# Kernel optimization log

Measured on AMD Instinct MI355X. Metric: run time of the kernel, lower is better.

## Reference

```python
import jax, jax.numpy as jnp
import numpy as np

N = 100_000      # nodes
M = 200_000      # hyperedges
E = 1_000_000    # incidence pairs
D_IN = 64
HEADS, D_OUT = 8, 16   # linear out = 8*16 = 128


def setup_inputs() -> dict:
    key = jax.random.key(0)
    k = jax.random.split(key, 7)
    X = jax.random.normal(k[0], (N, D_IN), dtype=jnp.float32)
    vertex = jax.random.randint(k[1], (E,), 0, N, dtype=jnp.int32)
    edges = jax.random.randint(k[2], (E,), 0, M, dtype=jnp.int32)
    dege = jax.random.uniform(k[3], (M, 1), dtype=jnp.float32)
    degv = jax.random.uniform(k[4], (N, 1), dtype=jnp.float32)
    W = jax.random.normal(k[5], (D_IN, HEADS * D_OUT), dtype=jnp.float32) / np.sqrt(D_IN)
    b = jax.random.normal(k[6], (HEADS * D_OUT,), dtype=jnp.float32) * 0.01
    return {"X": X, "vertex": vertex, "edges": edges, "dege": dege, "degv": degv, "W": W, "b": b}


def reference(X, vertex, edges, dege, degv, W, b):
    n_nodes = X.shape[0]
    n_edges = dege.shape[0]
    # vertex -> hyperedge aggregation (first_aggregate = 'mean')
    Xve = X[vertex]                                               # [E, D]
    sums = jax.ops.segment_sum(Xve, edges, num_segments=n_edges)  # [M, D]
    counts = jax.ops.segment_sum(jnp.ones((edges.shape[0],), X.dtype), edges, num_segments=n_edges)
    Xe = sums / jnp.maximum(counts, 1.0)[:, None]                 # empty edges -> 0
    Xe = Xe * dege
    # hyperedge -> vertex aggregation (sum)
    Xev = Xe[edges]                                               # [E, D]
    Xv = jax.ops.segment_sum(Xev, vertex, num_segments=n_nodes)   # [N, D]
    Xv = Xv * degv
    # normalize_l2: row norm is computed on a DETACHED tensor in torch
    rownorm = jnp.linalg.norm(jax.lax.stop_gradient(Xv), axis=1, keepdims=True)
    scale = jnp.where(rownorm > 0, 1.0 / rownorm, 0.0)
    Xn = Xv * scale
    return Xn @ W + b
```

## Files before the change

### kernel.cpp

```cpp
#include <hip/hip_runtime.h>


#define DIN 64
#define DOUT 128
#define CH 4096
#define BSHIFT 9
#define FINE 512
#define PAYBITS 18
#define PAYMASK ((1u << PAYBITS) - 1u)
#define XB 256

typedef float f32x4 __attribute__((ext_vector_type(4)));
typedef short bf16x8 __attribute__((ext_vector_type(8)));

__device__ __forceinline__ unsigned short f2b(float f) {
  unsigned u = __float_as_uint(f);
  u = u + 0x7fffu + ((u >> 16) & 1u);
  return (unsigned short)(u >> 16);
}
__device__ __forceinline__ float b2f(unsigned s) {
  return __uint_as_float(s << 16);
}

__global__ __launch_bounds__(256) void k_p1(
    const int* __restrict__ vertex, const int* __restrict__ edges,
    int* __restrict__ G, const float* __restrict__ X,
    unsigned short* __restrict__ Xb, int* __restrict__ done,
    int E, int BKE, int BK, int NCH, int total4) {
  if (blockIdx.x == 0 && threadIdx.x == 0) *done = 0;
  if (blockIdx.x >= (unsigned)NCH) {
    int xb = blockIdx.x - NCH;
    for (int i = xb * 256 + threadIdx.x; i < total4; i += XB * 256) {
      float4 a = ((const float4*)X)[i];
      ushort4 r;
      r.x = f2b(a.x); r.y = f2b(a.y); r.z = f2b(a.z); r.w = f2b(a.w);
      ((ushort4*)Xb)[i] = r;
    }
    return;
  }
  __shared__ int h[1024];
  for (int i = threadIdx.x; i < BK; i += 256) h[i] = 0;
  __syncthreads();
  int c = blockIdx.x;
  int s = c * CH, e_ = min(E, s + CH);
  for (int i = s + threadIdx.x; i < e_; i += 256) {
    atomicAdd(&h[edges[i] >> BSHIFT], 1);
    atomicAdd(&h[BKE + (vertex[i] >> BSHIFT)], 1);
  }
  __syncthreads();
  for (int b = threadIdx.x; b < BK; b += 256) G[(size_t)b * NCH + c] = h[b];
}

__global__ __launch_bounds__(256) void k_p1b(
    int* __restrict__ G, int* __restrict__ rowTot, int* __restrict__ bucketBase,
    int* __restrict__ done, int NCH, int BK) {
  int b = blockIdx.x;
  int* row = G + (size_t)b * NCH;
  __shared__ int wsum[4];
  __shared__ int carry;
  __shared__ bool amLast;
  if (threadIdx.x == 0) carry = 0;
  __syncthreads();
  for (int base = 0; base < NCH; base += 256) {
    int i = base + threadIdx.x;
    int v = (i < NCH) ? row[i] : 0;
    int lane = threadIdx.x & 63, wid = threadIdx.x >> 6;
    int inc = v;
    #pragma unroll
    for (int o = 1; o < 64; o <<= 1) {
      int t = __shfl_up(inc, o);
      if (lane >= o) inc += t;
    }
    if (lane == 63) wsum[wid] = inc;
    __syncthreads();
    int woff = carry;
    for (int w = 0; w < wid; ++w) woff += wsum[w];
    int excl = woff + inc - v;
    if (i < NCH) row[i] = excl;
    __syncthreads();
    if (threadIdx.x == 0) carry += wsum[0] + wsum[1] + wsum[2] + wsum[3];
    __syncthreads();
  }
  if (threadIdx.x == 0) {
    rowTot[b] = carry;
    __threadfence();
    amLast = (atomicAdd(done, 1) == gridDim.x - 1);
  }
  __syncthreads();
  if (!amLast) return;

  if (threadIdx.x == 0) carry = 0;
  __syncthreads();
  for (int base = 0; base < BK; base += 256) {
    int i = base + threadIdx.x;
    int v = (i < BK) ? atomicAdd(&rowTot[i], 0) : 0;
    int lane = threadIdx.x & 63, wid = threadIdx.x >> 6;
    int inc = v;
    #pragma unroll
    for (int o = 1; o < 64; o <<= 1) {
      int t = __shfl_up(inc, o);
      if (lane >= o) inc += t;
    }
    if (lane == 63) wsum[wid] = inc;
    __syncthreads();
    int woff = carry;
    for (int w = 0; w < wid; ++w) woff += wsum[w];
    int excl = woff + inc - v;
    if (i < BK) bucketBase[i] = excl;
    __syncthreads();
    if (threadIdx.x == 0) carry += wsum[0] + wsum[1] + wsum[2] + wsum[3];
    __syncthreads();
  }
  if (threadIdx.x == 0) bucketBase[BK] = carry;
}

__global__ __launch_bounds__(256) void p2_scatter(
    const int* __restrict__ vertex, const int* __restrict__ edges,
    const int* __restrict__ G, const int* __restrict__ bucketBase,
    unsigned* __restrict__ temp, int E, int BKE, int BK, int NCH) {
  __shared__ int curs[1024];
  int c = blockIdx.x;
  for (int b = threadIdx.x; b < BK; b += 256)
    curs[b] = bucketBase[b] + G[(size_t)b * NCH + c];
  __syncthreads();
  int s = c * CH, e_ = min(E, s + CH);
  for (int i = s + threadIdx.x; i < e_; i += 256) {
    int e = edges[i], v = vertex[i];
    int pE = atomicAdd(&curs[e >> BSHIFT], 1);
    temp[pE] = ((unsigned)(e & (FINE - 1)) << PAYBITS) | (unsigned)v;
    int pV = atomicAdd(&curs[BKE + (v >> BSHIFT)], 1);
    temp[pV] = ((unsigned)(v & (FINE - 1)) << PAYBITS) | (unsigned)e;
  }
}

__global__ __launch_bounds__(256) void p3_sort(
    const unsigned* __restrict__ temp, const int* __restrict__ bucketBase,
    int* __restrict__ off, int* __restrict__ perm, int BKE, int M, int N) {
  __shared__ int hist[FINE];
  __shared__ int pos[FINE];
  __shared__ int wsum[4];
  int g = blockIdx.x;
  bool isE = g < BKE;
  int gg = isE ? g : g - BKE;
  int keyBase = gg << BSHIFT;
  int cap = isE ? M : N;
  int offBase = (isE ? 0 : M) + keyBase;
  int fineCount = min(FINE, cap - keyBase);
  int pairBase = bucketBase[g], pairEnd = bucketBase[g + 1];
  int cnt = pairEnd - pairBase;

  for (int i = threadIdx.x; i < FINE; i += 256) hist[i] = 0;
  __syncthreads();
  for (int i = threadIdx.x; i < cnt; i += 256)
    atomicAdd(&hist[temp[pairBase + i] >> PAYBITS], 1);
  __syncthreads();

  int t2 = threadIdx.x * 2;
  int a0 = hist[t2], a1 = hist[t2 + 1];
  int tsum = a0 + a1;
  int lane = threadIdx.x & 63, wid = threadIdx.x >> 6;
  int inc = tsum;
  #pragma unroll
  for (int o = 1; o < 64; o <<= 1) {
    int t = __shfl_up(inc, o);
    if (lane >= o) inc += t;
  }
  if (lane == 63) wsum[wid] = inc;
  __syncthreads();
  int woff = 0;
  for (int w = 0; w < wid; ++w) woff += wsum[w];
  int excl = woff + inc - tsum;
  pos[t2] = excl; pos[t2 + 1] = excl + a0;
  __syncthreads();

  for (int f = threadIdx.x; f < fineCount; f += 256)
    off[offBase + f] = pairBase + pos[f] + hist[f];
  for (int f = threadIdx.x; f < FINE; f += 256) pos[f] += pairBase;
  __syncthreads();

  for (int i = threadIdx.x; i < cnt; i += 256) {
    unsigned p = temp[pairBase + i];
    int q = atomicAdd(&pos[p >> PAYBITS], 1);
    perm[q] = (int)(p & PAYMASK);
  }
}


__global__ __launch_bounds__(256) void k_edge(
    const unsigned short* __restrict__ Xb, const int* __restrict__ off,
    const int* __restrict__ perm, const float* __restrict__ dege,
    unsigned short* __restrict__ Xe, int M) {
  long long gid = (long long)blockIdx.x * 256 + threadIdx.x;
  int wv = (int)(gid >> 6);
  int lane = threadIdx.x & 63;
  int g = lane >> 4, li = lane & 15;
  int e = wv * 4 + g;
  bool valid = e < M;
  int start = 0, end = 0;
  if (valid) { start = e ? off[e - 1] : 0; end = off[e]; }
  int deg = end - start;
  int myidx = (valid && li < deg) ? perm[start + li] : 0;
  int jmax = min(deg, 16);
  int jw = jmax;
  jw = max(jw, __shfl_xor(jw, 16));
  jw = max(jw, __shfl_xor(jw, 32));
  const uint2* X2 = (const uint2*)Xb;
  float4 acc = make_float4(0.f, 0.f, 0.f, 0.f);
  #pragma unroll 4
  for (int j = 0; j < jw; ++j) {
    int v0 = __shfl(myidx, (g << 4) + j);
    if (j < jmax) {
      uint2 a = X2[(size_t)v0 * 16 + li];
      acc.x += b2f(a.x & 0xffffu); acc.y += b2f(a.x >> 16);
      acc.z += b2f(a.y & 0xffffu); acc.w += b2f(a.y >> 16);
    }
  }
  for (int j = 16; j < deg; ++j) {
    int v0 = perm[start + j];
    uint2 a = X2[(size_t)v0 * 16 + li];
    acc.x += b2f(a.x & 0xffffu); acc.y += b2f(a.x >> 16);
    acc.z += b2f(a.y & 0xffffu); acc.w += b2f(a.y >> 16);
  }
  if (valid) {
    float s = dege[e] / fmaxf((float)deg, 1.0f);
    ushort4 r;
    r.x = f2b(acc.x * s); r.y = f2b(acc.y * s);
    r.z = f2b(acc.z * s); r.w = f2b(acc.w * s);
    ((ushort4*)Xe)[(size_t)e * 16 + li] = r;
  }
}

__global__ __launch_bounds__(256) void k_nodeagg(
    const unsigned short* __restrict__ Xe, const int* __restrict__ off,
    const int* __restrict__ perm, const float* __restrict__ degv,
    unsigned short* __restrict__ xn, int N, int M) {
  long long gid = (long long)blockIdx.x * 256 + threadIdx.x;
  int wv = (int)(gid >> 6);
  int lane = threadIdx.x & 63;
  int g = lane >> 4, li = lane & 15;
  int node = wv * 4 + g;
  bool valid = node < N;
  int start = 0, end = 0;
  if (valid) { start = off[M + node - 1]; end = off[M + node]; }
  int deg = end - start;
  int myidx = (valid && li < deg) ? perm[start + li] : 0;
  int jmax = min(deg, 16);
  int jw = jmax;
  jw = max(jw, __shfl_xor(jw, 16));
  jw = max(jw, __shfl_xor(jw, 32));
  const uint2* Xe2 = (const uint2*)Xe;
  float4 acc = make_float4(0.f, 0.f, 0.f, 0.f);
  #pragma unroll 4
  for (int j = 0; j < jw; ++j) {
    int e0 = __shfl(myidx, (g << 4) + j);
    if (j < jmax) {
      uint2 a = Xe2[(size_t)e0 * 16 + li];
      acc.x += b2f(a.x & 0xffffu); acc.y += b2f(a.x >> 16);
      acc.z += b2f(a.y & 0xffffu); acc.w += b2f(a.y >> 16);
    }
  }
  for (int j = 16; j < deg; ++j) {
    int e0 = perm[start + j];
    uint2 a = Xe2[(size_t)e0 * 16 + li];
    acc.x += b2f(a.x & 0xffffu); acc.y += b2f(a.x >> 16);
    acc.z += b2f(a.y & 0xffffu); acc.w += b2f(a.y >> 16);
  }
  float dv = valid ? degv[node] : 0.f;
  acc.x *= dv; acc.y *= dv; acc.z *= dv; acc.w *= dv;
  float ss = acc.x * acc.x + acc.y * acc.y + acc.z * acc.z + acc.w * acc.w;
  #pragma unroll
  for (int o = 1; o <= 8; o <<= 1) ss += __shfl_xor(ss, o);
  float sc = ss > 0.0f ? 1.0f / sqrtf(ss) : 0.0f;
  if (valid) {
    ushort4 r;
    r.x = f2b(acc.x * sc); r.y = f2b(acc.y * sc);
    r.z = f2b(acc.z * sc); r.w = f2b(acc.w * sc);
    ((ushort4*)xn)[(size_t)node * 16 + li] = r;
  }
}

#define WPAD 72
__global__ __launch_bounds__(256) void k_linear(
    const unsigned short* __restrict__ xn, const float* __restrict__ W,
    const float* __restrict__ bias, float* __restrict__ out, int N) {
  __shared__ unsigned short Wt[DOUT * WPAD];
  for (int i = threadIdx.x; i < DIN * DOUT; i += 256) {
    int k = i >> 7, c = i & 127;
    Wt[c * WPAD + k] = f2b(W[i]);
  }
  __syncthreads();
  int lane = threadIdx.x & 63;
  int wid = threadIdx.x >> 6;
  int r = lane & 15, h = lane >> 4;

  bf16x8 Bf[8][2];
  #pragma unroll
  for (int c = 0; c < 8; ++c) {
    #pragma unroll
    for (int ks = 0; ks < 2; ++ks) {
      int col = c * 16 + r;
      int k0 = ks * 32 + h * 8;
      Bf[c][ks] = *(const bf16x8*)&Wt[col * WPAD + k0];
    }
  }
  float bcol[8];
  #pragma unroll
  for (int c = 0; c < 8; ++c) bcol[c] = bias[c * 16 + r];

  int strips = (N + 15) >> 4;
  for (int s = blockIdx.x * 4 + wid; s < strips; s += gridDim.x * 4) {
    int row0 = s << 4;
    const unsigned short* xrow = xn + (size_t)(row0 + r) * DIN;
    bf16x8 a0 = *(const bf16x8*)&xrow[h * 8];
    bf16x8 a1 = *(const bf16x8*)&xrow[32 + h * 8];
    #pragma unroll
    for (int c = 0; c < 8; ++c) {
      f32x4 acc = {bcol[c], bcol[c], bcol[c], bcol[c]};
      acc = __builtin_amdgcn_mfma_f32_16x16x32_bf16(a0, Bf[c][0], acc, 0, 0, 0);
      acc = __builtin_amdgcn_mfma_f32_16x16x32_bf16(a1, Bf[c][1], acc, 0, 0, 0);
      #pragma unroll
      for (int q = 0; q < 4; ++q)
        out[(size_t)(row0 + h * 4 + q) * DOUT + c * 16 + r] = acc[q];
    }
  }
}

extern "C" void kernel_launch(void* const* d_in, const int* in_sizes, int n_in,
                              void* d_out, int out_size, void* d_ws, size_t ws_size,
                              hipStream_t stream) {
  const float* X      = (const float*)d_in[0];
  const int*   vertex = (const int*)d_in[1];
  const int*   edges  = (const int*)d_in[2];
  const float* dege   = (const float*)d_in[3];
  const float* degv   = (const float*)d_in[4];
  const float* W      = (const float*)d_in[5];
  const float* b      = (const float*)d_in[6];
  float* out = (float*)d_out;

  int N = in_sizes[0] / DIN;
  int E = in_sizes[1];
  int M = in_sizes[3];

  int NCH = (E + CH - 1) / CH;
  int BKE = (M + FINE - 1) >> BSHIFT;
  int BKV = (N + FINE - 1) >> BSHIFT;
  int BK  = BKE + BKV;

  unsigned short* Xe = (unsigned short*)d_ws;
  unsigned short* Xb = Xe + (size_t)M * DIN;
  int*   off  = (int*)(Xb + (size_t)N * DIN);
  int*   perm = off + (M + N);
  char*  R    = (char*)(perm + 2 * (size_t)E);
  unsigned*       temp = (unsigned*)R;
  unsigned short* xn   = (unsigned short*)R;
  size_t rBytes = (size_t)2 * E * 4;
  size_t xBytes = (size_t)N * DIN * 2;
  char*  R2   = R + (rBytes > xBytes ? rBytes : xBytes);
  int*   G    = (int*)R2;
  int*   rowTot = G + (size_t)BK * NCH;
  int*   bucketBase = rowTot + BK;
  int*   done = bucketBase + BK + 1;

  int total4 = N * DIN / 4;
  k_p1<<<NCH + XB, 256, 0, stream>>>(vertex, edges, G, X, Xb, done,
                                     E, BKE, BK, NCH, total4);
  k_p1b<<<BK, 256, 0, stream>>>(G, rowTot, bucketBase, done, NCH, BK);
  p2_scatter<<<NCH, 256, 0, stream>>>(vertex, edges, G, bucketBase, temp,
                                      E, BKE, BK, NCH);
  p3_sort<<<BK, 256, 0, stream>>>(temp, bucketBase, off, perm, BKE, M, N);

  int edgeBlocks = (M + 15) / 16;
  k_edge<<<edgeBlocks, 256, 0, stream>>>(Xb, off, perm, dege, Xe, M);

  int nodeBlocks = (N + 15) / 16;
  k_nodeagg<<<nodeBlocks, 256, 0, stream>>>(Xe, off, perm, degv, xn, N, M);

  int strips = (N + 15) >> 4;
  int linBlocks = (strips + 3) / 4;
  k_linear<<<linBlocks, 256, 0, stream>>>(xn, W, b, out, N);
}
```

Before: 147.4 us.

## Fuse node aggregation with linear layer and widen edge gather

Node aggregation now writes normalized rows to shared memory and runs the MFMA projection in the same kernel. This removes the separate linear kernel and the round trip of the normalized matrix through global memory. W is pre-converted to bf16 by an extra block in the first kernel. The edge kernel now uses 8 lanes per edge with 16-byte loads instead of 16 lanes with 8-byte loads, and the histogram loop reads indices as int4. In exchange, each fused block reloads W fragments from global memory, and the workspace is no longer aliased, so it grows.

```diff
diff --git a/kernel.cpp b/kernel.cpp
--- a/kernel.cpp
+++ b/kernel.cpp
@@ -25,9 +25,17 @@
 __global__ __launch_bounds__(256) void k_p1(
     const int* __restrict__ vertex, const int* __restrict__ edges,
     int* __restrict__ G, const float* __restrict__ X,
-    unsigned short* __restrict__ Xb, int* __restrict__ done,
+    unsigned short* __restrict__ Xb, const float* __restrict__ W,
+    unsigned short* __restrict__ Wbf, int* __restrict__ done,
     int E, int BKE, int BK, int NCH, int total4) {
   if (blockIdx.x == 0 && threadIdx.x == 0) *done = 0;
+  if (blockIdx.x >= (unsigned)(NCH + XB)) {
+    for (int i = threadIdx.x; i < DIN * DOUT; i += 256) {
+      int k = i >> 7, c = i & 127;
+      Wbf[c * DIN + k] = f2b(W[i]);
+    }
+    return;
+  }
   if (blockIdx.x >= (unsigned)NCH) {
     int xb = blockIdx.x - NCH;
     for (int i = xb * 256 + threadIdx.x; i < total4; i += XB * 256) {
@@ -43,7 +51,17 @@
   __syncthreads();
   int c = blockIdx.x;
   int s = c * CH, e_ = min(E, s + CH);
-  for (int i = s + threadIdx.x; i < e_; i += 256) {
+  int n4 = (e_ - s) >> 2;
+  const int4* ep = (const int4*)(edges + s);
+  const int4* vp = (const int4*)(vertex + s);
+  for (int i = threadIdx.x; i < n4; i += 256) {
+    int4 ee = ep[i], vv = vp[i];
+    atomicAdd(&h[ee.x >> BSHIFT], 1); atomicAdd(&h[ee.y >> BSHIFT], 1);
+    atomicAdd(&h[ee.z >> BSHIFT], 1); atomicAdd(&h[ee.w >> BSHIFT], 1);
+    atomicAdd(&h[BKE + (vv.x >> BSHIFT)], 1); atomicAdd(&h[BKE + (vv.y >> BSHIFT)], 1);
+    atomicAdd(&h[BKE + (vv.z >> BSHIFT)], 1); atomicAdd(&h[BKE + (vv.w >> BSHIFT)], 1);
+  }
+  for (int i = s + (n4 << 2) + threadIdx.x; i < e_; i += 256) {
     atomicAdd(&h[edges[i] >> BSHIFT], 1);
     atomicAdd(&h[BKE + (vertex[i] >> BSHIFT)], 1);
   }
@@ -193,52 +211,62 @@
   long long gid = (long long)blockIdx.x * 256 + threadIdx.x;
   int wv = (int)(gid >> 6);
   int lane = threadIdx.x & 63;
-  int g = lane >> 4, li = lane & 15;
-  int e = wv * 4 + g;
+  int g = lane >> 3, li = lane & 7;
+  int e = wv * 8 + g;
   bool valid = e < M;
   int start = 0, end = 0;
   if (valid) { start = e ? off[e - 1] : 0; end = off[e]; }
   int deg = end - start;
   int myidx = (valid && li < deg) ? perm[start + li] : 0;
-  int jmax = min(deg, 16);
+  int jmax = min(deg, 8);
   int jw = jmax;
+  jw = max(jw, __shfl_xor(jw, 8));
   jw = max(jw, __shfl_xor(jw, 16));
   jw = max(jw, __shfl_xor(jw, 32));
-  const uint2* X2 = (const uint2*)Xb;
-  float4 acc = make_float4(0.f, 0.f, 0.f, 0.f);
+  const uint4* X4 = (const uint4*)Xb;
+  float acc[8] = {0.f, 0.f, 0.f, 0.f, 0.f, 0.f, 0.f, 0.f};
   #pragma unroll 4
   for (int j = 0; j < jw; ++j) {
-    int v0 = __shfl(myidx, (g << 4) + j);
+    int v0 = __shfl(myidx, (g << 3) + j);
     if (j < jmax) {
-      uint2 a = X2[(size_t)v0 * 16 + li];
-      acc.x += b2f(a.x & 0xffffu); acc.y += b2f(a.x >> 16);
-      acc.z += b2f(a.y & 0xffffu); acc.w += b2f(a.y >> 16);
-    }
-  }
-  for (int j = 16; j < deg; ++j) {
+      uint4 a = X4[(size_t)v0 * 8 + li];
+      acc[0] += b2f(a.x & 0xffffu); acc[1] += b2f(a.x >> 16);
+      acc[2] += b2f(a.y & 0xffffu); acc[3] += b2f(a.y >> 16);
+      acc[4] += b2f(a.z & 0xffffu); acc[5] += b2f(a.z >> 16);
+      acc[6] += b2f(a.w & 0xffffu); acc[7] += b2f(a.w >> 16);
+    }
+  }
+  for (int j = 8; j < deg; ++j) {
     int v0 = perm[start + j];
-    uint2 a = X2[(size_t)v0 * 16 + li];
-    acc.x += b2f(a.x & 0xffffu); acc.y += b2f(a.x >> 16);
-    acc.z += b2f(a.y & 0xffffu); acc.w += b2f(a.y >> 16);
+    uint4 a = X4[(size_t)v0 * 8 + li];
+    acc[0] += b2f(a.x & 0xffffu); acc[1] += b2f(a.x >> 16);
+    acc[2] += b2f(a.y & 0xffffu); acc[3] += b2f(a.y >> 16);
+    acc[4] += b2f(a.z & 0xffffu); acc[5] += b2f(a.z >> 16);
+    acc[6] += b2f(a.w & 0xffffu); acc[7] += b2f(a.w >> 16);
   }
   if (valid) {
     float s = dege[e] / fmaxf((float)deg, 1.0f);
-    ushort4 r;
-    r.x = f2b(acc.x * s); r.y = f2b(acc.y * s);
-    r.z = f2b(acc.z * s); r.w = f2b(acc.w * s);
-    ((ushort4*)Xe)[(size_t)e * 16 + li] = r;
-  }
-}
-
-__global__ __launch_bounds__(256) void k_nodeagg(
+    uint4 r;
+    r.x = (unsigned)f2b(acc[0] * s) | ((unsigned)f2b(acc[1] * s) << 16);
+    r.y = (unsigned)f2b(acc[2] * s) | ((unsigned)f2b(acc[3] * s) << 16);
+    r.z = (unsigned)f2b(acc[4] * s) | ((unsigned)f2b(acc[5] * s) << 16);
+    r.w = (unsigned)f2b(acc[6] * s) | ((unsigned)f2b(acc[7] * s) << 16);
+    ((uint4*)Xe)[(size_t)e * 8 + li] = r;
+  }
+}
+
+#define SPAD 72
+__global__ __launch_bounds__(256) void k_nodefused(
     const unsigned short* __restrict__ Xe, const int* __restrict__ off,
     const int* __restrict__ perm, const float* __restrict__ degv,
-    unsigned short* __restrict__ xn, int N, int M) {
-  long long gid = (long long)blockIdx.x * 256 + threadIdx.x;
-  int wv = (int)(gid >> 6);
+    const unsigned short* __restrict__ Wbf, const float* __restrict__ bias,
+    float* __restrict__ out, int N, int M) {
+  __shared__ __align__(16) unsigned short xnS[16][SPAD];
   int lane = threadIdx.x & 63;
+  int wv = threadIdx.x >> 6;
   int g = lane >> 4, li = lane & 15;
-  int node = wv * 4 + g;
+  int nodeIn = wv * 4 + g;
+  int node = blockIdx.x * 16 + nodeIn;
   bool valid = node < N;
   int start = 0, end = 0;
   if (valid) { start = off[M + node - 1]; end = off[M + node]; }
@@ -271,56 +299,30 @@
   #pragma unroll
   for (int o = 1; o <= 8; o <<= 1) ss += __shfl_xor(ss, o);
   float sc = ss > 0.0f ? 1.0f / sqrtf(ss) : 0.0f;
-  if (valid) {
-    ushort4 r;
-    r.x = f2b(acc.x * sc); r.y = f2b(acc.y * sc);
-    r.z = f2b(acc.z * sc); r.w = f2b(acc.w * sc);
-    ((ushort4*)xn)[(size_t)node * 16 + li] = r;
-  }
-}
-
-#define WPAD 72
-__global__ __launch_bounds__(256) void k_linear(
-    const unsigned short* __restrict__ xn, const float* __restrict__ W,
-    const float* __restrict__ bias, float* __restrict__ out, int N) {
-  __shared__ unsigned short Wt[DOUT * WPAD];
-  for (int i = threadIdx.x; i < DIN * DOUT; i += 256) {
-    int k = i >> 7, c = i & 127;
-    Wt[c * WPAD + k] = f2b(W[i]);
-  }
-  __syncthreads();
-  int lane = threadIdx.x & 63;
-  int wid = threadIdx.x >> 6;
+  ushort4 r4;
+  r4.x = f2b(acc.x * sc); r4.y = f2b(acc.y * sc);
+  r4.z = f2b(acc.z * sc); r4.w = f2b(acc.w * sc);
+  *(ushort4*)&xnS[nodeIn][li * 4] = r4;
+  __syncthreads();
+
   int r = lane & 15, h = lane >> 4;
-
-  bf16x8 Bf[8][2];
+  bf16x8 a0 = *(const bf16x8*)&xnS[r][h * 8];
+  bf16x8 a1 = *(const bf16x8*)&xnS[r][32 + h * 8];
+  int row0 = blockIdx.x * 16;
   #pragma unroll
-  for (int c = 0; c < 8; ++c) {
+  for (int cc = 0; cc < 2; ++cc) {
+    int c = wv * 2 + cc;
+    const unsigned short* wcol = Wbf + (size_t)(c * 16 + r) * DIN;
+    bf16x8 b0 = *(const bf16x8*)&wcol[h * 8];
+    bf16x8 b1 = *(const bf16x8*)&wcol[32 + h * 8];
+    float bc = bias[c * 16 + r];
+    f32x4 o4 = {bc, bc, bc, bc};
+    o4 = __builtin_amdgcn_mfma_f32_16x16x32_bf16(a0, b0, o4, 0, 0, 0);
+    o4 = __builtin_amdgcn_mfma_f32_16x16x32_bf16(a1, b1, o4, 0, 0, 0);
     #pragma unroll
-    for (int ks = 0; ks < 2; ++ks) {
-      int col = c * 16 + r;
-      int k0 = ks * 32 + h * 8;
-      Bf[c][ks] = *(const bf16x8*)&Wt[col * WPAD + k0];
-    }
-  }
-  float bcol[8];
-  #pragma unroll
-  for (int c = 0; c < 8; ++c) bcol[c] = bias[c * 16 + r];
-
-  int strips = (N + 15) >> 4;
-  for (int s = blockIdx.x * 4 + wid; s < strips; s += gridDim.x * 4) {
-    int row0 = s << 4;
-    const unsigned short* xrow = xn + (size_t)(row0 + r) * DIN;
-    bf16x8 a0 = *(const bf16x8*)&xrow[h * 8];
-    bf16x8 a1 = *(const bf16x8*)&xrow[32 + h * 8];
-    #pragma unroll
-    for (int c = 0; c < 8; ++c) {
-      f32x4 acc = {bcol[c], bcol[c], bcol[c], bcol[c]};
-      acc = __builtin_amdgcn_mfma_f32_16x16x32_bf16(a0, Bf[c][0], acc, 0, 0, 0);
-      acc = __builtin_amdgcn_mfma_f32_16x16x32_bf16(a1, Bf[c][1], acc, 0, 0, 0);
-      #pragma unroll
-      for (int q = 0; q < 4; ++q)
-        out[(size_t)(row0 + h * 4 + q) * DOUT + c * 16 + r] = acc[q];
+    for (int q = 0; q < 4; ++q) {
+      int row = row0 + h * 4 + q;
+      if (row < N) out[(size_t)row * DOUT + c * 16 + r] = o4[q];
     }
   }
 }
@@ -350,32 +352,26 @@
   unsigned short* Xb = Xe + (size_t)M * DIN;
   int*   off  = (int*)(Xb + (size_t)N * DIN);
   int*   perm = off + (M + N);
-  char*  R    = (char*)(perm + 2 * (size_t)E);
-  unsigned*       temp = (unsigned*)R;
-  unsigned short* xn   = (unsigned short*)R;
-  size_t rBytes = (size_t)2 * E * 4;
-  size_t xBytes = (size_t)N * DIN * 2;
-  char*  R2   = R + (rBytes > xBytes ? rBytes : xBytes);
-  int*   G    = (int*)R2;
+  unsigned* temp = (unsigned*)(perm + 2 * (size_t)E);
+  int*   G    = (int*)(temp + 2 * (size_t)E);
   int*   rowTot = G + (size_t)BK * NCH;
   int*   bucketBase = rowTot + BK;
   int*   done = bucketBase + BK + 1;
+  size_t wOff = (((size_t)(done + 1 - (int*)d_ws) * 4) + 15) & ~(size_t)15;
+  unsigned short* Wbf = (unsigned short*)((char*)d_ws + wOff);
 
   int total4 = N * DIN / 4;
-  k_p1<<<NCH + XB, 256, 0, stream>>>(vertex, edges, G, X, Xb, done,
-                                     E, BKE, BK, NCH, total4);
+  k_p1<<<NCH + XB + 1, 256, 0, stream>>>(vertex, edges, G, X, Xb, W, Wbf, done,
+                                         E, BKE, BK, NCH, total4);
   k_p1b<<<BK, 256, 0, stream>>>(G, rowTot, bucketBase, done, NCH, BK);
   p2_scatter<<<NCH, 256, 0, stream>>>(vertex, edges, G, bucketBase, temp,
                                       E, BKE, BK, NCH);
   p3_sort<<<BK, 256, 0, stream>>>(temp, bucketBase, off, perm, BKE, M, N);
 
-  int edgeBlocks = (M + 15) / 16;
+  int edgeBlocks = (M + 31) / 32;
   k_edge<<<edgeBlocks, 256, 0, stream>>>(Xb, off, perm, dege, Xe, M);
 
   int nodeBlocks = (N + 15) / 16;
-  k_nodeagg<<<nodeBlocks, 256, 0, stream>>>(Xe, off, perm, degv, xn, N, M);
-
-  int strips = (N + 15) >> 4;
-  int linBlocks = (strips + 3) / 4;
-  k_linear<<<linBlocks, 256, 0, stream>>>(xn, W, b, out, N);
-}
+  k_nodefused<<<nodeBlocks, 256, 0, stream>>>(Xe, off, perm, degv, Wbf, b,
+                                              out, N, M);
+}
```

Result: faster. 138.6 us (-6.0%).
